# Kernel optimization log

Measured on AMD Instinct MI355X. Metric: run time of the kernel, lower is better.

Reference implementation:

```python
import jax, jax.numpy as jnp
import numpy as np

N = 262144      # number of nodes in steady-state graph
E = 4_000_000   # number of existing edges
B = 16384       # update batch size
F = 15          # node/edge feature dim (hardcoded in setup())


def setup_inputs() -> dict:
    key = jax.random.key(0)
    k1, k2, k3, k4, k5, k6, k7 = jax.random.split(key, 7)
    # node IDs are sorted/unique (slot i holds ID i); this matches G.idx lookup semantics
    G_idx = jnp.arange(N, dtype=jnp.int32)
    G_x = jax.random.normal(k1, (N, F), dtype=jnp.float32)
    edge_index = jax.random.randint(k2, (2, E), 0, N, dtype=jnp.int32)  # [2,E] node slots
    edge_attr = jax.random.normal(k3, (E, F), dtype=jnp.float32)
    # steady-state hot path: updated (src,dst) pairs are existing edges, unique per batch
    sel = jax.random.choice(k4, E, (B,), replace=False)
    srcID = G_idx[edge_index[0, sel]]
    dstID = G_idx[edge_index[1, sel]]
    src_feature = jax.random.normal(k5, (B, F), dtype=jnp.float32)
    dst_feature = jax.random.normal(k6, (B, F), dtype=jnp.float32)
    edge_feature = jax.random.normal(k7, (B, F), dtype=jnp.float32)
    return {"G_x": G_x, "G_idx": G_idx, "edge_index": edge_index, "edge_attr": edge_attr,
            "srcID": srcID, "dstID": dstID, "src_feature": src_feature,
            "dst_feature": dst_feature, "edge_feature": edge_feature}


def reference(G_x, G_idx, edge_index, edge_attr, srcID, dstID,
              src_feature, dst_feature, edge_feature):
    n_nodes, feat = G_x.shape
    n_edges = edge_attr.shape[0]
    b = srcID.shape[0]

    # ---- update_nodes: the python loop writes src then dst for each row i, so the
    ids = jnp.stack([srcID, dstID], axis=1).reshape(-1)                  # [2B]
    feats = jnp.stack([src_feature, dst_feature], axis=1).reshape(-1, feat)  # [2B,F]
    slots = jnp.searchsorted(G_idx, ids).astype(jnp.int32)              # ID -> node slot
    order = jnp.arange(2 * b, dtype=jnp.int32)
    last = jnp.full((n_nodes,), -1, dtype=jnp.int32).at[slots].max(order)  # last writer per node
    hit = last >= 0
    x_new = jnp.where(hit[:, None], feats[jnp.clip(last, 0)], G_x)
    updated = hit  # == torch.isin(G.idx, unique(cat([srcID,dstID])))

    # ---- update_edges: find_edge_indices via sorted edge keys + searchsorted
    src_slot = jnp.searchsorted(G_idx, srcID)
    dst_slot = jnp.searchsorted(G_idx, dstID)
    ekeys = edge_index[0].astype(jnp.int64) * n_nodes + edge_index[1].astype(jnp.int64)
    qkeys = src_slot.astype(jnp.int64) * n_nodes + dst_slot.astype(jnp.int64)
    eorder = jnp.argsort(ekeys)
    esorted = ekeys[eorder]
    pos = jnp.clip(jnp.searchsorted(esorted, qkeys), 0, n_edges - 1)
    found = esorted[pos] == qkeys
    eidx = jnp.where(found, eorder[pos], n_edges)  # n_edges == OOB -> dropped
    edge_attr_new = edge_attr.at[eidx].set(edge_feature, mode='drop')

    # process() returns (G.x, G.edge_index, G.edge_attr); floats concatenated for a
    # single dense output, edge_index unchanged in the steady-state path.
    out = jnp.concatenate([x_new, edge_attr_new], axis=0)  # [N+E, F]
    return out, updated, edge_index
```

## Files before the change

kernel.cpp:

```cpp
#include <hip/hip_runtime.h>
#include <stdint.h>

#define HASH_EMPTY 0xFFFFFFFFFFFFFFFFULL
#define RES_EMPTY  0x7FFFFFFF

__device__ __forceinline__ uint32_t hash_key(uint64_t k) {
    k *= 0x9E3779B97F4A7C15ULL;
    return (uint32_t)(k >> 32);
}

__global__ void init_kernel(int* __restrict__ last, unsigned long long* __restrict__ hkeys,
                            int* __restrict__ res, int N, int H, int B) {
    int t = blockIdx.x * blockDim.x + threadIdx.x;
    if (t < N) last[t] = -1;
    if (t < H) hkeys[t] = HASH_EMPTY;
    if (t < B) res[t] = RES_EMPTY;
}

__global__ void writes_kernel(const int* __restrict__ srcID, const int* __restrict__ dstID,
                              int* __restrict__ last, unsigned long long* __restrict__ hkeys,
                              int* __restrict__ hvals, int B, int N, int H) {
    int i = blockIdx.x * blockDim.x + threadIdx.x;
    if (i < 2 * B) {
        int id = (i & 1) ? dstID[i >> 1] : srcID[i >> 1];
        atomicMax(&last[id], i);
    }
    if (i < B) {
        uint64_t key = (uint64_t)(uint32_t)srcID[i] * (uint32_t)N + (uint32_t)dstID[i];
        uint32_t h = hash_key(key) & (uint32_t)(H - 1);
        while (true) {
            unsigned long long old = atomicCAS(&hkeys[h], HASH_EMPTY, (unsigned long long)key);
            if (old == HASH_EMPTY || old == (unsigned long long)key) { hvals[h] = i; break; }
            h = (h + 1) & (uint32_t)(H - 1);
        }
    }
}

__global__ void edge_pass_kernel(const int* __restrict__ edge_index, float* __restrict__ out_ei,
                                 const unsigned long long* __restrict__ hkeys,
                                 const int* __restrict__ hvals, int* __restrict__ res,
                                 long long E, int N, int H) {
    long long stride = (long long)gridDim.x * blockDim.x;
    for (long long e = (long long)blockIdx.x * blockDim.x + threadIdx.x; e < E; e += stride) {
        int s = edge_index[e];
        int d = edge_index[E + e];
        out_ei[e]     = (float)s;
        out_ei[E + e] = (float)d;
        uint64_t key = (uint64_t)(uint32_t)s * (uint32_t)N + (uint32_t)d;
        uint32_t h = hash_key(key) & (uint32_t)(H - 1);
        while (true) {
            unsigned long long k = hkeys[h];
            if (k == HASH_EMPTY) break;
            if (k == (unsigned long long)key) { atomicMin(&res[hvals[h]], (int)e); break; }
            h = (h + 1) & (uint32_t)(H - 1);
        }
    }
}

__global__ void scatter_kernel(const float* __restrict__ edge_feature, const int* __restrict__ res,
                               float* __restrict__ out_edge, int B, int F) {
    int t = blockIdx.x * blockDim.x + threadIdx.x;
    if (t >= B * F) return;
    int q = t / F;
    int f = t - q * F;
    int e = res[q];
    if (e == RES_EMPTY) return;
    out_edge[(long long)e * F + f] = edge_feature[t];
}

__global__ void nodes_kernel(const float* __restrict__ G_x, const float* __restrict__ srcf,
                             const float* __restrict__ dstf, const int* __restrict__ last,
                             float* __restrict__ out_x, float* __restrict__ out_upd,
                             int N, int F) {
    int t = blockIdx.x * blockDim.x + threadIdx.x;
    int NF = N * F;
    if (t < NF) {
        int n = t / 15;
        if (F != 15) n = t / F;
        int f = t - n * F;
        int l = last[n];
        float v;
        if (l >= 0) {
            const float* row = (l & 1) ? dstf : srcf;
            v = row[(l >> 1) * F + f];
        } else {
            v = G_x[t];
        }
        out_x[t] = v;
    } else if (t < NF + N) {
        int n = t - NF;
        out_upd[n] = (last[n] >= 0) ? 1.0f : 0.0f;
    }
}

extern "C" void kernel_launch(void* const* d_in, const int* in_sizes, int n_in,
                              void* d_out, int out_size, void* d_ws, size_t ws_size,
                              hipStream_t stream) {
    const float* G_x         = (const float*)d_in[0];
    const int*   edge_index  = (const int*)d_in[2];
    const float* edge_attr   = (const float*)d_in[3];
    const int*   srcID       = (const int*)d_in[4];
    const int*   dstID       = (const int*)d_in[5];
    const float* src_feature = (const float*)d_in[6];
    const float* dst_feature = (const float*)d_in[7];
    const float* edge_feature= (const float*)d_in[8];

    const int       N = in_sizes[1];
    const long long E = (long long)in_sizes[2] / 2;
    const int       B = in_sizes[4];
    const int       F = in_sizes[0] / N;
    const int       H = 65536;

    float* out      = (float*)d_out;
    float* out_x    = out;
    float* out_edge = out + (long long)N * F;
    float* out_upd  = out + (long long)(N + E) * F;
    float* out_ei   = out_upd + N;

    char* ws = (char*)d_ws;
    int* last = (int*)ws;                         ws += (size_t)N * sizeof(int);
    unsigned long long* hkeys = (unsigned long long*)ws; ws += (size_t)H * sizeof(unsigned long long);
    int* hvals = (int*)ws;                        ws += (size_t)H * sizeof(int);
    int* res = (int*)ws;

    const int T = 256;
    int initN = N > H ? N : H; if (B > initN) initN = B;

    hipLaunchKernelGGL(init_kernel, dim3((initN + T - 1) / T), dim3(T), 0, stream,
                       last, hkeys, res, N, H, B);
    hipLaunchKernelGGL(writes_kernel, dim3((2 * B + T - 1) / T), dim3(T), 0, stream,
                       srcID, dstID, last, hkeys, hvals, B, N, H);
    hipMemcpyAsync(out_edge, edge_attr, (size_t)E * F * sizeof(float),
                   hipMemcpyDeviceToDevice, stream);
    hipLaunchKernelGGL(edge_pass_kernel, dim3(2048), dim3(T), 0, stream,
                       edge_index, out_ei, hkeys, hvals, res, E, N, H);
    hipLaunchKernelGGL(scatter_kernel, dim3((B * F + T - 1) / T), dim3(T), 0, stream,
                       edge_feature, res, out_edge, B, F);
    hipLaunchKernelGGL(nodes_kernel, dim3(((long long)N * (F + 1) + T - 1) / T), dim3(T), 0, stream,
                       G_x, src_feature, dst_feature, last, out_x, out_upd, N, F);
}
```

Measured before the change: 534.1 us.

## Fuse edge_attr copy into vectorized edge pass and merge scatter/node kernels

Replaces the device-to-device memcpy of edge_attr with a float4 grid-stride copy inside the edge hash-probe kernel. That kernel now also reads edge_index as int4 and probes four edges per thread. The scatter and node-update kernels are merged into one finalize kernel. The aim is to cut launch and serialization overhead and to overlap the bulk copy with the latency-bound hash probing. In exchange, the copy assumes 16-byte alignment and an element count divisible by four, and the single kernel with three roles may balance work less evenly across threads.

```diff
diff --git a/kernel.cpp b/kernel.cpp
--- a/kernel.cpp
+++ b/kernel.cpp
@@ -36,12 +36,43 @@
     }
 }
 
-__global__ void edge_pass_kernel(const int* __restrict__ edge_index, float* __restrict__ out_ei,
+__global__ void edge_mega_kernel(const float4* __restrict__ ea4, float4* __restrict__ oe4,
+                                 long long CP4,
+                                 const int* __restrict__ edge_index, float* __restrict__ out_ei,
                                  const unsigned long long* __restrict__ hkeys,
                                  const int* __restrict__ hvals, int* __restrict__ res,
                                  long long E, int N, int H) {
-    long long stride = (long long)gridDim.x * blockDim.x;
-    for (long long e = (long long)blockIdx.x * blockDim.x + threadIdx.x; e < E; e += stride) {
+    const long long stride = (long long)gridDim.x * blockDim.x;
+    const long long tid = (long long)blockIdx.x * blockDim.x + threadIdx.x;
+
+    for (long long i = tid; i < CP4; i += stride) oe4[i] = ea4[i];
+
+    const long long E4 = E >> 2;
+    const int4* ei_s4 = (const int4*)edge_index;
+    const int4* ei_d4 = (const int4*)(edge_index + E);
+    float4* oei_s4 = (float4*)out_ei;
+    float4* oei_d4 = (float4*)(out_ei + E);
+    for (long long i = tid; i < E4; i += stride) {
+        int4 s = ei_s4[i];
+        int4 d = ei_d4[i];
+        oei_s4[i] = make_float4((float)s.x, (float)s.y, (float)s.z, (float)s.w);
+        oei_d4[i] = make_float4((float)d.x, (float)d.y, (float)d.z, (float)d.w);
+        const long long e = i << 2;
+        const int ss[4] = {s.x, s.y, s.z, s.w};
+        const int dd[4] = {d.x, d.y, d.z, d.w};
+        #pragma unroll
+        for (int j = 0; j < 4; ++j) {
+            uint64_t key = (uint64_t)(uint32_t)ss[j] * (uint32_t)N + (uint32_t)dd[j];
+            uint32_t h = hash_key(key) & (uint32_t)(H - 1);
+            while (true) {
+                unsigned long long k = hkeys[h];
+                if (k == HASH_EMPTY) break;
+                if (k == (unsigned long long)key) { atomicMin(&res[hvals[h]], (int)(e + j)); break; }
+                h = (h + 1) & (uint32_t)(H - 1);
+            }
+        }
+    }
+    for (long long e = (E4 << 2) + tid; e < E; e += stride) {
         int s = edge_index[e];
         int d = edge_index[E + e];
         out_ei[e]     = (float)s;
@@ -57,38 +88,34 @@
     }
 }
 
-__global__ void scatter_kernel(const float* __restrict__ edge_feature, const int* __restrict__ res,
-                               float* __restrict__ out_edge, int B, int F) {
-    int t = blockIdx.x * blockDim.x + threadIdx.x;
-    if (t >= B * F) return;
-    int q = t / F;
-    int f = t - q * F;
-    int e = res[q];
-    if (e == RES_EMPTY) return;
-    out_edge[(long long)e * F + f] = edge_feature[t];
-}
-
-__global__ void nodes_kernel(const float* __restrict__ G_x, const float* __restrict__ srcf,
-                             const float* __restrict__ dstf, const int* __restrict__ last,
-                             float* __restrict__ out_x, float* __restrict__ out_upd,
-                             int N, int F) {
-    int t = blockIdx.x * blockDim.x + threadIdx.x;
-    int NF = N * F;
-    if (t < NF) {
-        int n = t / 15;
-        if (F != 15) n = t / F;
-        int f = t - n * F;
+__global__ void finalize_kernel(const float* __restrict__ G_x, const float* __restrict__ srcf,
+                                const float* __restrict__ dstf, const int* __restrict__ last,
+                                const float* __restrict__ edge_feature, const int* __restrict__ res,
+                                float* __restrict__ out_x, float* __restrict__ out_upd,
+                                float* __restrict__ out_edge, int N, int F, int B) {
+    const int t = blockIdx.x * blockDim.x + threadIdx.x;
+    const int SC = B * F;
+    const int NF = N * F;
+    if (t < SC) {
+        int q = (F == 15) ? (t / 15) : (t / F);
+        int f = t - q * F;
+        int e = res[q];
+        if (e != RES_EMPTY) out_edge[(long long)e * F + f] = edge_feature[t];
+    } else if (t < SC + NF) {
+        int u = t - SC;
+        int n = (F == 15) ? (u / 15) : (u / F);
+        int f = u - n * F;
         int l = last[n];
         float v;
         if (l >= 0) {
             const float* row = (l & 1) ? dstf : srcf;
             v = row[(l >> 1) * F + f];
         } else {
-            v = G_x[t];
+            v = G_x[u];
         }
-        out_x[t] = v;
-    } else if (t < NF + N) {
-        int n = t - NF;
+        out_x[u] = v;
+    } else if (t < SC + NF + N) {
+        int n = t - SC - NF;
         out_upd[n] = (last[n] >= 0) ? 1.0f : 0.0f;
     }
 }
@@ -130,12 +157,15 @@
                        last, hkeys, res, N, H, B);
     hipLaunchKernelGGL(writes_kernel, dim3((2 * B + T - 1) / T), dim3(T), 0, stream,
                        srcID, dstID, last, hkeys, hvals, B, N, H);
-    hipMemcpyAsync(out_edge, edge_attr, (size_t)E * F * sizeof(float),
-                   hipMemcpyDeviceToDevice, stream);
-    hipLaunchKernelGGL(edge_pass_kernel, dim3(2048), dim3(T), 0, stream,
+
+    const long long EF = E * (long long)F;
+    const long long CP4 = EF >> 2;
+    hipLaunchKernelGGL(edge_mega_kernel, dim3(2048), dim3(T), 0, stream,
+                       (const float4*)edge_attr, (float4*)out_edge, CP4,
                        edge_index, out_ei, hkeys, hvals, res, E, N, H);
-    hipLaunchKernelGGL(scatter_kernel, dim3((B * F + T - 1) / T), dim3(T), 0, stream,
-                       edge_feature, res, out_edge, B, F);
-    hipLaunchKernelGGL(nodes_kernel, dim3(((long long)N * (F + 1) + T - 1) / T), dim3(T), 0, stream,
-                       G_x, src_feature, dst_feature, last, out_x, out_upd, N, F);
+
+    const long long FIN = (long long)B * F + (long long)N * F + N;
+    hipLaunchKernelGGL(finalize_kernel, dim3((FIN + T - 1) / T), dim3(T), 0, stream,
+                       G_x, src_feature, dst_feature, last, edge_feature, res,
+                       out_x, out_upd, out_edge, N, F, B);
 }
```

After: 534.9 us. No clear change (+0.1%).
